# Optimization experiments

Measured on AMD Instinct MI355X. Metric: run time of the kernel, lower is better.

Reference implementation:

```python
import jax, jax.numpy as jnp
import numpy as np

B, N, D, H = 32, 1024, 512, 8

def setup_inputs() -> dict:
    key = jax.random.key(0)
    ks = jax.random.split(key, 11)
    std = D ** (-0.5)
    inp = {
        'k': jax.random.normal(ks[0], (B, N, D), jnp.float32),
        'v': jax.random.normal(ks[1], (B, N, D), jnp.float32),
        'q': jax.random.normal(ks[2], (B, N, D), jnp.float32),
        # per-head Linear weights, torch layout (out, in), stacked over heads
        'Wk': jax.random.normal(ks[3], (H, D, D), jnp.float32) * std,
        'bk': jax.random.uniform(ks[4], (H, D), jnp.float32, -std, std),
        'Wv': jax.random.normal(ks[5], (H, D, D), jnp.float32) * std,
        'bv': jax.random.uniform(ks[6], (H, D), jnp.float32, -std, std),
        'Wq': jax.random.normal(ks[7], (H, D, D), jnp.float32) * std,
        'bq': jax.random.uniform(ks[8], (H, D), jnp.float32, -std, std),
        # output projection: (hidden, n_heads*hidden)
        'Wo': jax.random.normal(ks[9], (D, H * D), jnp.float32) * (H * D) ** (-0.5),
        'bo': jax.random.uniform(ks[10], (D,), jnp.float32, -(H * D) ** (-0.5), (H * D) ** (-0.5)),
    }
    return inp

def reference(k, v, q, Wk, bk, Wv, bv, Wq, bq, Wo, bo):
    # Batched per-head projections (torch Linear: y = x @ W.T + b)
    kh = jnp.einsum('bnd,hed->bhne', k, Wk) + bk[:, None, :]  # [B,H,N,D]
    vh = jnp.einsum('bnd,hed->bhne', v, Wv) + bv[:, None, :]
    qh = jnp.einsum('bnd,hed->bhne', q, Wq) + bq[:, None, :]
    scale = jnp.asarray(qh.shape[-1] ** 0.5, qh.dtype)
    scores = jnp.einsum('bhjd,bhid->bhij', kh, qh) / scale      # [B,H,Nq,Nk]
    w = jax.nn.softmax(scores, axis=-1)
    out = jnp.einsum('bhij,bhjd->bhid', w, vh)                  # [B,H,Nq,D]
    # torch stacks heads on last dim then flattens: out[..., d, h] -> d*H + h
    cat = out.transpose(0, 2, 3, 1).reshape(out.shape[0], out.shape[2], -1)  # [B,Nq,D*H]
    rep = cat @ Wo.T + bo                                        # [B,Nq,D]
    return rep
```

## Files before the change

kernel.cpp:

```cpp
#include <hip/hip_runtime.h>
#include <hip/hip_bf16.h>
#include <cstdint>
#include <type_traits>

constexpr int B_SZ = 32;
constexpr int N_SZ = 1024;
constexpr int D_SZ = 512;
constexpr int H_SZ = 8;
constexpr int HD   = H_SZ * D_SZ;

typedef __attribute__((ext_vector_type(8))) short short8;
typedef __attribute__((ext_vector_type(4))) float floatx4;
typedef unsigned short u16;

static __device__ __forceinline__ u16 f2bf(float f) {
    union { float f; unsigned int i; } c; c.f = f;
    unsigned int x = c.i;
    unsigned int r = x + 0x7FFFu + ((x >> 16) & 1u);
    return (u16)(r >> 16);
}

__global__ void cvt_kernel(const float* __restrict__ src, u16* __restrict__ dst) {
    int idx = (blockIdx.x * 256 + threadIdx.x) * 4;
    float4 v = *(const float4*)(src + idx);
    ushort4 o;
    o.x = f2bf(v.x); o.y = f2bf(v.y); o.z = f2bf(v.z); o.w = f2bf(v.w);
    *(ushort4*)(dst + idx) = o;
}

__global__ void woperm_kernel(const float* __restrict__ Wo, u16* __restrict__ Wp) {
    int idx = blockIdx.x * 256 + threadIdx.x;
    int e = idx >> 12;
    int c = idx & 4095;
    int d  = c & 511;
    int hh = c >> 9;
    Wp[idx] = f2bf(Wo[((size_t)e << 12) + d * H_SZ + hh]);
}

template<typename AT, int OM>
__global__ __launch_bounds__(256, 2)
void gemm_bt(const AT* __restrict__ A, const u16* __restrict__ W,
             const float* __restrict__ bias, void* __restrict__ Cout,
             int M, int Nc, int K)
{
    __shared__ u16 Alds[128 * 40];
    __shared__ u16 Blds[128 * 40];
    const int tid  = threadIdx.x;
    const int lane = tid & 63;
    const int wave = tid >> 6;
    const int wm = wave >> 1, wn = wave & 1;
    const int m16 = lane & 15, quad = lane >> 4;
    const size_t tm0 = (size_t)blockIdx.x * 128;
    const size_t tn0 = (size_t)blockIdx.y * 128;

    floatx4 acc[4][4];
#pragma unroll
    for (int i = 0; i < 4; i++)
#pragma unroll
        for (int j = 0; j < 4; j++) acc[i][j] = (floatx4){0.f, 0.f, 0.f, 0.f};

    const int srow  = tid >> 1;
    const int skoff = (tid & 1) * 16;
    const AT*  ag = A + (tm0 + srow) * (size_t)K + skoff;
    const u16* bg = W + (tn0 + srow) * (size_t)K + skoff;

    for (int k0 = 0; k0 < K; k0 += 32) {
        short8 a0, a1;
        if constexpr (std::is_same_v<AT, float>) {
            float4 f0 = *(const float4*)(ag + k0);
            float4 f1 = *(const float4*)(ag + k0 + 4);
            float4 f2 = *(const float4*)(ag + k0 + 8);
            float4 f3 = *(const float4*)(ag + k0 + 12);
            a0 = (short8){(short)f2bf(f0.x), (short)f2bf(f0.y), (short)f2bf(f0.z), (short)f2bf(f0.w),
                          (short)f2bf(f1.x), (short)f2bf(f1.y), (short)f2bf(f1.z), (short)f2bf(f1.w)};
            a1 = (short8){(short)f2bf(f2.x), (short)f2bf(f2.y), (short)f2bf(f2.z), (short)f2bf(f2.w),
                          (short)f2bf(f3.x), (short)f2bf(f3.y), (short)f2bf(f3.z), (short)f2bf(f3.w)};
        } else {
            a0 = *(const short8*)(ag + k0);
            a1 = *(const short8*)(ag + k0 + 8);
        }
        short8 b0 = *(const short8*)(bg + k0);
        short8 b1 = *(const short8*)(bg + k0 + 8);
        __syncthreads();
        *(short8*)&Alds[srow * 40 + skoff]     = a0;
        *(short8*)&Alds[srow * 40 + skoff + 8] = a1;
        *(short8*)&Blds[srow * 40 + skoff]     = b0;
        *(short8*)&Blds[srow * 40 + skoff + 8] = b1;
        __syncthreads();
        short8 af[4], bf[4];
#pragma unroll
        for (int t = 0; t < 4; t++) {
            af[t] = *(const short8*)&Alds[(wm * 64 + t * 16 + m16) * 40 + quad * 8];
            bf[t] = *(const short8*)&Blds[(wn * 64 + t * 16 + m16) * 40 + quad * 8];
        }
#pragma unroll
        for (int i = 0; i < 4; i++)
#pragma unroll
            for (int j = 0; j < 4; j++)
                acc[i][j] = __builtin_amdgcn_mfma_f32_16x16x32_bf16(af[i], bf[j], acc[i][j], 0, 0, 0);
    }

#pragma unroll
    for (int j = 0; j < 4; j++) {
        int col = (int)tn0 + wn * 64 + j * 16 + m16;
        float bsv = bias[col];
#pragma unroll
        for (int i = 0; i < 4; i++) {
            size_t row = tm0 + wm * 64 + i * 16 + quad * 4;
            if constexpr (OM == 2) {
                int cloc = (int)(row >> 10);
                int n0   = (int)(row & 1023);
                ushort4 pk;
                pk.x = f2bf(acc[i][j][0] + bsv);
                pk.y = f2bf(acc[i][j][1] + bsv);
                pk.z = f2bf(acc[i][j][2] + bsv);
                pk.w = f2bf(acc[i][j][3] + bsv);
                u16* vtp = (u16*)Cout;
                *(ushort4*)&vtp[((size_t)cloc * HD + col) * N_SZ + n0] = pk;
            } else {
#pragma unroll
                for (int r = 0; r < 4; r++) {
                    if constexpr (OM == 1)
                        ((float*)Cout)[(row + r) * (size_t)Nc + col] = acc[i][j][r] + bsv;
                    else
                        ((u16*)Cout)[(row + r) * (size_t)Nc + col] = f2bf(acc[i][j][r] + bsv);
                }
            }
        }
    }
}

__global__ __launch_bounds__(256, 2)
void attn_kernel(const u16* __restrict__ qh, const u16* __restrict__ kh,
                 const u16* __restrict__ vt, u16* __restrict__ ao)
{
    __shared__ u16 Klds[32 * 512];
    __shared__ u16 Vtlds[512 * 32];
    u16* Plds = Klds;

    const int tid  = threadIdx.x;
    const int lane = tid & 63;
    const int wave = tid >> 6;
    const int m16  = lane & 15;
    const int quad = lane >> 4;
    const int qt = blockIdx.x;
    const int h  = blockIdx.y;
    const int bb = blockIdx.z;

    const int kxor = m16 & 7;
    const int qx8  = (quad ^ (kxor & 3)) * 8;
    const int kx32 = (kxor & 4) * 8;
    const u16* kaddrE = &Klds[m16 * 512 + qx8 + kx32];
    const u16* kaddrO = &Klds[m16 * 512 + qx8 - kx32];
    const int vx8 = (quad ^ (m16 & 3) ^ ((m16 >> 2) & 3)) * 8;
    const u16* vaddr = &Vtlds[m16 * 32 + vx8];
    const int ebase = wave * 16 + (lane >> 2);
    const int cw8   = ((lane & 3) ^ ((lane >> 2) & 3) ^ ((lane >> 4) & 3)) * 8;

    const int qrow = qt * 64 + wave * 16 + m16;
    const u16* qptr = qh + ((size_t)(bb * N_SZ + qrow)) * HD + h * D_SZ + quad * 8;
    short8 qfrag[16];
#pragma unroll
    for (int kk = 0; kk < 16; kk++)
        qfrag[kk] = *(const short8*)(qptr + kk * 32);

    floatx4 acc[32];
#pragma unroll
    for (int i = 0; i < 32; i++) acc[i] = (floatx4){0.f, 0.f, 0.f, 0.f};
    float mrow[4], lrow[4];
#pragma unroll
    for (int r = 0; r < 4; r++) { mrow[r] = -3.0e38f; lrow[r] = 0.f; }

    const float scale = 0.04419417382415922f;
    const u16* kbase  = kh + ((size_t)(bb * N_SZ)) * HD + h * D_SZ;
    const u16* vtbase = vt + ((size_t)bb * HD + h * D_SZ) * N_SZ;

    short8 kreg[8];
#pragma unroll
    for (int i = 0; i < 8; i++) {
        int row = i * 4 + wave;
        kreg[i] = *(const short8*)(kbase + (size_t)row * HD + lane * 8);
    }

    for (int kt = 0; kt < 32; kt++) {
        __syncthreads();
#pragma unroll
        for (int i = 0; i < 8; i++) {
            int row = i * 4 + wave;
            int cp  = lane ^ (row & 7);
            *(short8*)&Klds[row * 512 + cp * 8] = kreg[i];
        }
        __syncthreads();

        short8 vreg[8];
#pragma unroll
        for (int i = 0; i < 8; i++) {
            int e = i * 64 + ebase;
            vreg[i] = *(const short8*)(vtbase + (size_t)e * N_SZ + kt * 32 + (lane & 3) * 8);
        }

        floatx4 s0 = (floatx4){0.f,0.f,0.f,0.f}, s1 = (floatx4){0.f,0.f,0.f,0.f};
#pragma unroll
        for (int kk = 0; kk < 16; kk++) {
            const u16* p = (kk & 1) ? kaddrO : kaddrE;
            short8 kb0 = *(const short8*)(p + kk * 32);
            short8 kb1 = *(const short8*)(p + kk * 32 + 8192);
            s0 = __builtin_amdgcn_mfma_f32_16x16x32_bf16(qfrag[kk], kb0, s0, 0, 0, 0);
            s1 = __builtin_amdgcn_mfma_f32_16x16x32_bf16(qfrag[kk], kb1, s1, 0, 0, 0);
        }

        float alpha[4];
        u16 pbits[8];
#pragma unroll
        for (int r = 0; r < 4; r++) {
            float a0 = s0[r] * scale, a1 = s1[r] * scale;
            float t = fmaxf(a0, a1);
#pragma unroll
            for (int msk = 1; msk <= 8; msk <<= 1) t = fmaxf(t, __shfl_xor(t, msk, 64));
            float mnew = fmaxf(mrow[r], t);
            alpha[r] = __expf(mrow[r] - mnew);
            mrow[r] = mnew;
            float p0 = __expf(a0 - mnew), p1 = __expf(a1 - mnew);
            float ps = p0 + p1;
#pragma unroll
            for (int msk = 1; msk <= 8; msk <<= 1) ps += __shfl_xor(ps, msk, 64);
            lrow[r] = lrow[r] * alpha[r] + ps;
            pbits[r]     = f2bf(p0);
            pbits[4 + r] = f2bf(p1);
        }

#pragma unroll
        for (int i = 0; i < 8; i++) {
            int e = i * 64 + ebase;
            *(short8*)&Vtlds[e * 32 + cw8] = vreg[i];
        }
        __syncthreads();

#pragma unroll
        for (int r = 0; r < 4; r++) {
            Plds[wave * 640 + (quad * 4 + r) * 40 + m16]      = pbits[r];
            Plds[wave * 640 + (quad * 4 + r) * 40 + 16 + m16] = pbits[4 + r];
        }

        float amin = fminf(fminf(alpha[0], alpha[1]), fminf(alpha[2], alpha[3]));
        if (__any(amin < 1.0f)) {
#pragma unroll
            for (int ct = 0; ct < 32; ct++)
#pragma unroll
                for (int r = 0; r < 4; r++) acc[ct][r] *= alpha[r];
        }

        int ktn = (kt < 31) ? (kt + 1) : kt;
#pragma unroll
        for (int i = 0; i < 8; i++) {
            int row = i * 4 + wave;
            kreg[i] = *(const short8*)(kbase + (size_t)(ktn * 32 + row) * HD + lane * 8);
        }

        short8 pf = *(const short8*)&Plds[wave * 640 + m16 * 40 + quad * 8];
#pragma unroll
        for (int ct = 0; ct < 32; ct++) {
            short8 vf = *(const short8*)(vaddr + ct * 512);
            acc[ct] = __builtin_amdgcn_mfma_f32_16x16x32_bf16(pf, vf, acc[ct], 0, 0, 0);
        }
    }

#pragma unroll
    for (int r = 0; r < 4; r++) {
        int row = qt * 64 + wave * 16 + quad * 4 + r;
        float invl = 1.0f / lrow[r];
        size_t obase = ((size_t)(bb * N_SZ + row)) * HD + h * D_SZ;
#pragma unroll
        for (int ct = 0; ct < 32; ct++)
            ao[obase + ct * 16 + m16] = f2bf(acc[ct][r] * invl);
    }
}

extern "C" void kernel_launch(void* const* d_in, const int* in_sizes, int n_in,
                              void* d_out, int out_size, void* d_ws, size_t ws_size,
                              hipStream_t stream)
{
    const float* kin = (const float*)d_in[0];
    const float* vin = (const float*)d_in[1];
    const float* qin = (const float*)d_in[2];
    const float* Wk  = (const float*)d_in[3];
    const float* bk  = (const float*)d_in[4];
    const float* Wv  = (const float*)d_in[5];
    const float* bv  = (const float*)d_in[6];
    const float* Wq  = (const float*)d_in[7];
    const float* bq  = (const float*)d_in[8];
    const float* Wo  = (const float*)d_in[9];
    const float* bo  = (const float*)d_in[10];
    float* out = (float*)d_out;

    u16* ws = (u16*)d_ws;
    const size_t wEl      = (size_t)H_SZ * D_SZ * D_SZ;
    const size_t permEl   = (size_t)D_SZ * HD;
    const size_t perBatch = (size_t)N_SZ * HD;
    const size_t fixedEl  = 3 * wEl + permEl;
    long long availEl = (long long)(ws_size / 2) - (long long)fixedEl;
    int C = 1;
    if (availEl > 0) {
        long long c = availEl / (long long)(4 * perBatch);
        C = (int)(c < 1 ? 1 : (c > B_SZ ? B_SZ : c));
    }

    u16* wqb = ws;
    u16* wkb = wqb + wEl;
    u16* wvb = wkb + wEl;
    u16* wop = wvb + wEl;
    u16* qh  = wop + permEl;
    u16* khb = qh  + (size_t)C * perBatch;
    u16* vtb = khb + (size_t)C * perBatch;
    u16* ao  = vtb + (size_t)C * perBatch;

    const int cvtBlocks = (int)(wEl / 1024);
    cvt_kernel<<<cvtBlocks, 256, 0, stream>>>(Wq, wqb);
    cvt_kernel<<<cvtBlocks, 256, 0, stream>>>(Wk, wkb);
    cvt_kernel<<<cvtBlocks, 256, 0, stream>>>(Wv, wvb);
    woperm_kernel<<<(int)(permEl / 256), 256, 0, stream>>>(Wo, wop);

    for (int b0 = 0; b0 < B_SZ; b0 += C) {
        int Cc = (B_SZ - b0 < C) ? (B_SZ - b0) : C;
        int M = Cc * N_SZ;
        dim3 gp(M / 128, HD / 128);
        gemm_bt<float, 0><<<gp, 256, 0, stream>>>(qin + (size_t)b0 * N_SZ * D_SZ, wqb, bq, qh,  M, HD, D_SZ);
        gemm_bt<float, 0><<<gp, 256, 0, stream>>>(kin + (size_t)b0 * N_SZ * D_SZ, wkb, bk, khb, M, HD, D_SZ);
        gemm_bt<float, 2><<<gp, 256, 0, stream>>>(vin + (size_t)b0 * N_SZ * D_SZ, wvb, bv, vtb, M, HD, D_SZ);
        attn_kernel<<<dim3(N_SZ / 64, H_SZ, Cc), 256, 0, stream>>>(qh, khb, vtb, ao);
        gemm_bt<u16, 1><<<dim3(M / 128, D_SZ / 128), 256, 0, stream>>>(ao, wop, bo,
                                                                       out + (size_t)b0 * N_SZ * D_SZ, M, D_SZ, HD);
    }
}
```

Baseline: 3.608 ms.

## Restructure attention PV split across waves, lazy rescale, swizzled block order

Reworks the attention kernel so that each wave computes output for all 64 query rows over a 128-column slice of the value dimension, instead of 16 rows over all 512 columns. Each V fragment read from LDS is now reused across four MFMAs, and the P tile plus per-row alpha values are shared through LDS. It also transposes the QK MFMA so each lane holds one query row, adds a lazy max update that only rescales when the max grows by more than a threshold, and uses packed bf16 conversion and s_setprio around MFMA loops. Block indices are swizzled for XCD locality, and the sync points and K prefetch are reordered. The costs are extra LDS traffic for alpha and flags and a reliance on a threshold-based softmax rescale.

```diff
diff --git a/kernel.cpp b/kernel.cpp
--- a/kernel.cpp
+++ b/kernel.cpp
@@ -12,12 +12,19 @@
 typedef __attribute__((ext_vector_type(8))) short short8;
 typedef __attribute__((ext_vector_type(4))) float floatx4;
 typedef unsigned short u16;
+typedef unsigned int   u32;
 
 static __device__ __forceinline__ u16 f2bf(float f) {
     union { float f; unsigned int i; } c; c.f = f;
     unsigned int x = c.i;
     unsigned int r = x + 0x7FFFu + ((x >> 16) & 1u);
     return (u16)(r >> 16);
+}
+
+static __device__ __forceinline__ u32 cvt_pk_bf16(float a, float b) {
+    u32 r;
+    asm("v_cvt_pk_bf16_f32 %0, %1, %2" : "=v"(r) : "v"(a), "v"(b));
+    return r;
 }
 
 __global__ void cvt_kernel(const float* __restrict__ src, u16* __restrict__ dst) {
@@ -136,16 +143,23 @@
 {
     __shared__ u16 Klds[32 * 512];
     __shared__ u16 Vtlds[512 * 32];
-    u16* Plds = Klds;
+    u16*   Pov    = Klds;
+    float* alphaF = (float*)&Klds[2560];
+    float* lF     = (float*)&Klds[2688];
+    u32*   flagp  = (u32*)&Klds[2816];
 
     const int tid  = threadIdx.x;
     const int lane = tid & 63;
     const int wave = tid >> 6;
     const int m16  = lane & 15;
     const int quad = lane >> 4;
-    const int qt = blockIdx.x;
-    const int h  = blockIdx.y;
-    const int bb = blockIdx.z;
+
+    const int orig = blockIdx.x + ((int)blockIdx.y << 4) + ((int)blockIdx.z << 7);
+    const int cpx  = ((int)gridDim.z << 7) >> 3;
+    const int swz  = (orig & 7) * cpx + (orig >> 3);
+    const int qt = swz & 15;
+    const int h  = (swz >> 4) & 7;
+    const int bb = swz >> 7;
 
     const int kxor = m16 & 7;
     const int qx8  = (quad ^ (kxor & 3)) * 8;
@@ -164,12 +178,13 @@
     for (int kk = 0; kk < 16; kk++)
         qfrag[kk] = *(const short8*)(qptr + kk * 32);
 
-    floatx4 acc[32];
-#pragma unroll
-    for (int i = 0; i < 32; i++) acc[i] = (floatx4){0.f, 0.f, 0.f, 0.f};
-    float mrow[4], lrow[4];
-#pragma unroll
-    for (int r = 0; r < 4; r++) { mrow[r] = -3.0e38f; lrow[r] = 0.f; }
+    floatx4 acc[8][4];
+#pragma unroll
+    for (int j = 0; j < 8; j++)
+#pragma unroll
+        for (int qc = 0; qc < 4; qc++) acc[j][qc] = (floatx4){0.f, 0.f, 0.f, 0.f};
+
+    float mrow = -3.0e38f, lrow = 0.f;
 
     const float scale = 0.04419417382415922f;
     const u16* kbase  = kh + ((size_t)(bb * N_SZ)) * HD + h * D_SZ;
@@ -199,80 +214,119 @@
             vreg[i] = *(const short8*)(vtbase + (size_t)e * N_SZ + kt * 32 + (lane & 3) * 8);
         }
 
-        floatx4 s0 = (floatx4){0.f,0.f,0.f,0.f}, s1 = (floatx4){0.f,0.f,0.f,0.f};
+        floatx4 s0a = (floatx4){0.f,0.f,0.f,0.f}, s0b = s0a, s1a = s0a, s1b = s0a;
+        __builtin_amdgcn_s_setprio(1);
 #pragma unroll
         for (int kk = 0; kk < 16; kk++) {
             const u16* p = (kk & 1) ? kaddrO : kaddrE;
             short8 kb0 = *(const short8*)(p + kk * 32);
             short8 kb1 = *(const short8*)(p + kk * 32 + 8192);
-            s0 = __builtin_amdgcn_mfma_f32_16x16x32_bf16(qfrag[kk], kb0, s0, 0, 0, 0);
-            s1 = __builtin_amdgcn_mfma_f32_16x16x32_bf16(qfrag[kk], kb1, s1, 0, 0, 0);
-        }
-
-        float alpha[4];
-        u16 pbits[8];
-#pragma unroll
-        for (int r = 0; r < 4; r++) {
-            float a0 = s0[r] * scale, a1 = s1[r] * scale;
-            float t = fmaxf(a0, a1);
-#pragma unroll
-            for (int msk = 1; msk <= 8; msk <<= 1) t = fmaxf(t, __shfl_xor(t, msk, 64));
-            float mnew = fmaxf(mrow[r], t);
-            alpha[r] = __expf(mrow[r] - mnew);
-            mrow[r] = mnew;
-            float p0 = __expf(a0 - mnew), p1 = __expf(a1 - mnew);
-            float ps = p0 + p1;
-#pragma unroll
-            for (int msk = 1; msk <= 8; msk <<= 1) ps += __shfl_xor(ps, msk, 64);
-            lrow[r] = lrow[r] * alpha[r] + ps;
-            pbits[r]     = f2bf(p0);
-            pbits[4 + r] = f2bf(p1);
-        }
+            if (kk & 1) {
+                s0b = __builtin_amdgcn_mfma_f32_16x16x32_bf16(kb0, qfrag[kk], s0b, 0, 0, 0);
+                s1b = __builtin_amdgcn_mfma_f32_16x16x32_bf16(kb1, qfrag[kk], s1b, 0, 0, 0);
+            } else {
+                s0a = __builtin_amdgcn_mfma_f32_16x16x32_bf16(kb0, qfrag[kk], s0a, 0, 0, 0);
+                s1a = __builtin_amdgcn_mfma_f32_16x16x32_bf16(kb1, qfrag[kk], s1a, 0, 0, 0);
+            }
+        }
+        __builtin_amdgcn_s_setprio(0);
+        floatx4 s0 = s0a + s0b;
+        floatx4 s1 = s1a + s1b;
+
+        float a[8];
+#pragma unroll
+        for (int r = 0; r < 4; r++) { a[r] = s0[r] * scale; a[4 + r] = s1[r] * scale; }
+        float pm = fmaxf(fmaxf(fmaxf(a[0], a[1]), fmaxf(a[2], a[3])),
+                         fmaxf(fmaxf(a[4], a[5]), fmaxf(a[6], a[7])));
+        pm = fmaxf(pm, __shfl_xor(pm, 16, 64));
+        pm = fmaxf(pm, __shfl_xor(pm, 32, 64));
+        float alpha = 1.0f;
+        u32 wflag = 0u;
+        if (__any(pm > mrow + 8.0f)) {
+            float mnew = fmaxf(mrow, pm);
+            alpha = __expf(mrow - mnew);
+            mrow = mnew;
+            wflag = 1u;
+        }
+        float p[8];
+        float ps = 0.f;
+#pragma unroll
+        for (int i = 0; i < 8; i++) { p[i] = __expf(a[i] - mrow); ps += p[i]; }
+        ps += __shfl_xor(ps, 16, 64);
+        ps += __shfl_xor(ps, 32, 64);
+        lrow = lrow * alpha + ps;
+
+        u32 w0 = cvt_pk_bf16(p[0], p[1]);
+        u32 w1 = cvt_pk_bf16(p[2], p[3]);
+        u32 w2 = cvt_pk_bf16(p[4], p[5]);
+        u32 w3 = cvt_pk_bf16(p[6], p[7]);
+
+        int ktn = (kt < 31) ? (kt + 1) : kt;
+#pragma unroll
+        for (int i = 0; i < 8; i++) {
+            int row = i * 4 + wave;
+            kreg[i] = *(const short8*)(kbase + (size_t)(ktn * 32 + row) * HD + lane * 8);
+        }
+
+        __syncthreads();
 
 #pragma unroll
         for (int i = 0; i < 8; i++) {
             int e = i * 64 + ebase;
             *(short8*)&Vtlds[e * 32 + cw8] = vreg[i];
         }
-        __syncthreads();
-
+        {
+            int q40 = (wave * 16 + m16) * 40;
+            uint2 lo; lo.x = w0; lo.y = w1;
+            uint2 hi; hi.x = w2; hi.y = w3;
+            *(uint2*)&Pov[q40 + quad * 4]      = lo;
+            *(uint2*)&Pov[q40 + 16 + quad * 4] = hi;
+        }
+        if (quad == 0) alphaF[wave * 16 + m16] = alpha;
+        if (lane == 0) flagp[wave] = wflag;
+        __syncthreads();
+
+        u32 f = flagp[0] | flagp[1] | flagp[2] | flagp[3];
+        if (f) {
+#pragma unroll
+            for (int qc = 0; qc < 4; qc++) {
+#pragma unroll
+                for (int r = 0; r < 4; r++) {
+                    float av = alphaF[qc * 16 + quad * 4 + r];
+#pragma unroll
+                    for (int j = 0; j < 8; j++) acc[j][qc][r] *= av;
+                }
+            }
+        }
+
+        short8 pf[4];
+#pragma unroll
+        for (int qc = 0; qc < 4; qc++)
+            pf[qc] = *(const short8*)&Pov[(qc * 16 + m16) * 40 + quad * 8];
+        __builtin_amdgcn_s_setprio(1);
+#pragma unroll
+        for (int j = 0; j < 8; j++) {
+            short8 vf = *(const short8*)(vaddr + (wave * 8 + j) * 512);
+#pragma unroll
+            for (int qc = 0; qc < 4; qc++)
+                acc[j][qc] = __builtin_amdgcn_mfma_f32_16x16x32_bf16(pf[qc], vf, acc[j][qc], 0, 0, 0);
+        }
+        __builtin_amdgcn_s_setprio(0);
+    }
+
+    if (quad == 0) lF[wave * 16 + m16] = lrow;
+    __syncthreads();
+#pragma unroll
+    for (int qc = 0; qc < 4; qc++) {
 #pragma unroll
         for (int r = 0; r < 4; r++) {
-            Plds[wave * 640 + (quad * 4 + r) * 40 + m16]      = pbits[r];
-            Plds[wave * 640 + (quad * 4 + r) * 40 + 16 + m16] = pbits[4 + r];
-        }
-
-        float amin = fminf(fminf(alpha[0], alpha[1]), fminf(alpha[2], alpha[3]));
-        if (__any(amin < 1.0f)) {
-#pragma unroll
-            for (int ct = 0; ct < 32; ct++)
-#pragma unroll
-                for (int r = 0; r < 4; r++) acc[ct][r] *= alpha[r];
-        }
-
-        int ktn = (kt < 31) ? (kt + 1) : kt;
-#pragma unroll
-        for (int i = 0; i < 8; i++) {
-            int row = i * 4 + wave;
-            kreg[i] = *(const short8*)(kbase + (size_t)(ktn * 32 + row) * HD + lane * 8);
-        }
-
-        short8 pf = *(const short8*)&Plds[wave * 640 + m16 * 40 + quad * 8];
-#pragma unroll
-        for (int ct = 0; ct < 32; ct++) {
-            short8 vf = *(const short8*)(vaddr + ct * 512);
-            acc[ct] = __builtin_amdgcn_mfma_f32_16x16x32_bf16(pf, vf, acc[ct], 0, 0, 0);
-        }
-    }
-
-#pragma unroll
-    for (int r = 0; r < 4; r++) {
-        int row = qt * 64 + wave * 16 + quad * 4 + r;
-        float invl = 1.0f / lrow[r];
-        size_t obase = ((size_t)(bb * N_SZ + row)) * HD + h * D_SZ;
-#pragma unroll
-        for (int ct = 0; ct < 32; ct++)
-            ao[obase + ct * 16 + m16] = f2bf(acc[ct][r] * invl);
+            int row = qt * 64 + qc * 16 + quad * 4 + r;
+            float invl = 1.0f / lF[qc * 16 + quad * 4 + r];
+            size_t obase = ((size_t)(bb * N_SZ + row)) * HD + h * D_SZ + wave * 128;
+#pragma unroll
+            for (int j = 0; j < 8; j++)
+                ao[obase + j * 16 + m16] = f2bf(acc[j][qc][r] * invl);
+        }
     }
 }
 
```

Measured after the change: 2.965 ms. -17.8%, faster.
